# Optimization experiments

Hardware: AMD Instinct MI355X
Metric: run time of the kernel (lower is better)

The kernel has to match this reference:

```python
import jax, jax.numpy as jnp
import numpy as np

N = 50000      # nodes per type
E = 200000     # edges per relation
H, D = 4, 64   # heads, per-head dim
C = H * D      # hidden = hc_graph * heads = 256
L = 3          # num_hops (HGTConv layers)
HC_LIN, HC_TASK = 256, 128
OUT_DIMS = (3, 3, 3, 5, 1, 1, 8)  # ptr_l1/l2/l3, leaf_category, signed, floating, size


def setup_inputs() -> dict:
    key = jax.random.key(0)
    ks = jax.random.split(key, 24)
    f = lambda k, s: jax.random.normal(k, s, dtype=jnp.float32) * 0.05
    ri = lambda k: jax.random.randint(k, (E,), 0, N, dtype=jnp.int32)
    return {
        "xe": f(ks[0], (N, C)),
        "xs": f(ks[1], (N, C)),
        "ee_src": ri(ks[2]), "ee_dst": ri(ks[3]),
        "es_src": ri(ks[4]), "es_dst": ri(ks[5]),
        "se_src": ri(ks[6]), "se_dst": ri(ks[7]),
        # per-layer, per-node-type projections (2 node types)
        "Wk": f(ks[8], (L, 2, C, C)),
        "Wq": f(ks[9], (L, 2, C, C)),
        "Wv": f(ks[10], (L, 2, C, C)),
        "Wa": f(ks[11], (L, 2, C, C)),
        "skip": jnp.ones((L, 2), dtype=jnp.float32),
        # per-layer, per-relation attention/message transforms (3 relations)
        "Arel": f(ks[12], (L, 3, H, D, D)),
        "Mrel": f(ks[13], (L, 3, H, D, D)),
        "mu": jnp.ones((L, 3, H), dtype=jnp.float32),
        # shared linear stack + 7 task heads (final out padded to 8, sliced per head)
        "Wsh": f(ks[14], (2, HC_LIN, HC_LIN)),
        "bsh": jnp.zeros((2, HC_LIN), dtype=jnp.float32),
        "Wt1": f(ks[15], (7, HC_LIN, HC_TASK)),
        "bt1": jnp.zeros((7, HC_TASK), dtype=jnp.float32),
        "Wt2": f(ks[16], (7, HC_TASK, 8)),
        "bt2": jnp.zeros((7, 8), dtype=jnp.float32),
    }


def _seg_softmax(scores, seg, n):
    m = jax.ops.segment_max(scores, seg, num_segments=n)
    e = jnp.exp(scores - m[seg])
    s = jax.ops.segment_sum(e, seg, num_segments=n)
    return e / (s[seg] + 1e-16)


def _hgt_forward(xe, xs, ee_src, ee_dst, es_src, es_dst, se_src, se_dst,
                 Wk, Wq, Wv, Wa, skip, Arel, Mrel, mu, Wsh, bsh, Wt1, bt1, Wt2, bt2):
    inv_sqrt_d = 1.0 / jnp.sqrt(jnp.float32(D))

    def rel(k_src, v_src, q_dst, src, dst, A, M, m):
        kt = jnp.einsum('ehd,hdf->ehf', k_src[src], A)          # [E,H,D]
        score = (q_dst[dst] * kt).sum(-1) * (m * inv_sqrt_d)    # [E,H]
        msg = jnp.einsum('ehd,hdf->ehf', v_src[src], M)         # [E,H,D]
        return score, msg

    for l in range(L):
        ke = (xe @ Wk[l, 0]).reshape(N, H, D)
        qe = (xe @ Wq[l, 0]).reshape(N, H, D)
        ve = (xe @ Wv[l, 0]).reshape(N, H, D)
        ks_ = (xs @ Wk[l, 1]).reshape(N, H, D)
        qs = (xs @ Wq[l, 1]).reshape(N, H, D)
        vs = (xs @ Wv[l, 1]).reshape(N, H, D)

        s0, m0 = rel(ke, ve, qe, ee_src, ee_dst, Arel[l, 0], Mrel[l, 0], mu[l, 0])  # expr->expr
        s1, m1 = rel(ke, ve, qs, es_src, es_dst, Arel[l, 1], Mrel[l, 1], mu[l, 1])  # expr->stmt
        s2, m2 = rel(ks_, vs, qe, se_src, se_dst, Arel[l, 2], Mrel[l, 2], mu[l, 2])  # stmt->expr

        # destination 'expr': softmax over all incoming edges (rel0 + rel2)
        sc_e = jnp.concatenate([s0, s2], axis=0)
        ms_e = jnp.concatenate([m0, m2], axis=0)
        dst_e = jnp.concatenate([ee_dst, se_dst], axis=0)
        a_e = _seg_softmax(sc_e, dst_e, N)
        agg_e = jax.ops.segment_sum(a_e[..., None] * ms_e, dst_e, num_segments=N).reshape(N, C)

        # destination 'stmt': only rel1
        a_s = _seg_softmax(s1, es_dst, N)
        agg_s = jax.ops.segment_sum(a_s[..., None] * m1, es_dst, num_segments=N).reshape(N, C)

        be = jax.nn.sigmoid(skip[l, 0])
        bs = jax.nn.sigmoid(skip[l, 1])
        xe = be * (jax.nn.gelu(agg_e, approximate=False) @ Wa[l, 0]) + (1.0 - be) * xe
        xs = bs * (jax.nn.gelu(agg_s, approximate=False) @ Wa[l, 1]) + (1.0 - bs) * xs

    # shared linear stack on 'expr' nodes
    h = xe
    for i in range(Wsh.shape[0]):
        h = jax.nn.relu(h @ Wsh[i] + bsh[i])

    # 7 task heads: hidden layer + final (padded to 8 outputs, sliced per head)
    t = jax.nn.relu(jnp.einsum('nc,kct->knt', h, Wt1) + bt1[:, None, :])  # [7,N,HC_TASK]
    o = jnp.einsum('knt,kto->kno', t, Wt2) + bt2[:, None, :]              # [7,N,8]
    outs = [o[i, :, :d] for i, d in enumerate(OUT_DIMS)]
    return jnp.concatenate(outs, axis=-1)  # [N, 24]


def reference(xe, xs, ee_src, ee_dst, es_src, es_dst, se_src, se_dst,
              Wk, Wq, Wv, Wa, skip, Arel, Mrel, mu, Wsh, bsh, Wt1, bt1, Wt2, bt2):
    return _hgt_forward(xe, xs, ee_src, ee_dst, es_src, es_dst, se_src, se_dst,
                        Wk, Wq, Wv, Wa, skip, Arel, Mrel, mu, Wsh, bsh, Wt1, bt1, Wt2, bt2)
```

## Files before the change

### kernel.cpp

```cpp
#include <hip/hip_runtime.h>
#include <hip/hip_fp16.h>
#include <cmath>


#define CDIM 256
#define AR_R (256 * 256)

using f16x8 = __attribute__((ext_vector_type(8))) _Float16;
using f16x4 = __attribute__((ext_vector_type(4))) _Float16;
using f16x2 = __attribute__((ext_vector_type(2))) _Float16;
using f32x4 = __attribute__((ext_vector_type(4))) float;

__device__ __forceinline__ float gelu_f(float x) {
    return 0.5f * x * (1.0f + erff(x * 0.70710678118654752f));
}

__device__ __forceinline__ float dot4f(const f16x4 a, const f16x4 b) {
#if __has_builtin(__builtin_amdgcn_fdot2)
    f16x2 al = {a[0], a[1]}, ah = {a[2], a[3]};
    f16x2 bl = {b[0], b[1]}, bh = {b[2], b[3]};
    float r = __builtin_amdgcn_fdot2(al, bl, 0.0f, false);
    return __builtin_amdgcn_fdot2(ah, bh, r, false);
#else
    return (float)a[0] * (float)b[0] + (float)a[1] * (float)b[1] +
           (float)a[2] * (float)b[2] + (float)a[3] * (float)b[3];
#endif
}

__global__ __launch_bounds__(256) void zero_k(int* __restrict__ p, size_t n) {
    size_t i = (size_t)blockIdx.x * blockDim.x + threadIdx.x;
    const size_t stride = (size_t)gridDim.x * blockDim.x;
    for (; i < n; i += stride) p[i] = 0;
}

__global__ __launch_bounds__(256) void cvt_k(const float* __restrict__ in,
                                             _Float16* __restrict__ out,
                                             size_t n4) {
    size_t i = (size_t)blockIdx.x * blockDim.x + threadIdx.x;
    const size_t stride = (size_t)gridDim.x * blockDim.x;
    for (; i < n4; i += stride) {
        const float4 v = ((const float4*)in)[i];
        f16x4 o;
        o[0] = (_Float16)v.x; o[1] = (_Float16)v.y;
        o[2] = (_Float16)v.z; o[3] = (_Float16)v.w;
        ((f16x4*)out)[i] = o;
    }
}

__device__ __forceinline__ void cvtT_dev(const float* __restrict__ W,
                                         _Float16* __restrict__ dst) {
    const int o = blockIdx.x, c = threadIdx.x;
    dst[(size_t)o * 256 + c] = (_Float16)W[(size_t)c * 256 + o];
}

__device__ __forceinline__ void foldT_dev(const float* __restrict__ Wbase,
                                          const float* __restrict__ T,
                                          _Float16* __restrict__ dst) {
    __shared__ float row[256];
    const int c = blockIdx.x, t = threadIdx.x;
    row[t] = Wbase[(size_t)c * 256 + t];
    __syncthreads();
    const int h = t >> 6, f = t & 63;
    const float* Th = T + h * 4096;
    float acc = 0.f;
#pragma unroll 8
    for (int d = 0; d < 64; ++d) acc += row[h * 64 + d] * Th[d * 64 + f];
    dst[(size_t)t * 256 + c] = (_Float16)acc;
}

__global__ __launch_bounds__(256) void prep_layer_k(
    const float* __restrict__ Wk, const float* __restrict__ Wq,
    const float* __restrict__ Wv, const float* __restrict__ Wa,
    const float* __restrict__ Arel, const float* __restrict__ Mrel, int l,
    _Float16* __restrict__ arena) {
    const size_t CC = 65536, HDD = 16384;
    _Float16* L = arena + (size_t)l * 10 * AR_R;
    const float* Wk0 = Wk + (l * 2 + 0) * CC;
    const float* Wk1 = Wk + (l * 2 + 1) * CC;
    const float* Wv0 = Wv + (l * 2 + 0) * CC;
    const float* Wv1 = Wv + (l * 2 + 1) * CC;
    switch (blockIdx.y) {
        case 0: cvtT_dev(Wq + (l * 2 + 0) * CC, L); break;
        case 1: foldT_dev(Wk0, Arel + (l * 3 + 0) * HDD, L + 1 * AR_R); break;
        case 2: foldT_dev(Wk0, Arel + (l * 3 + 1) * HDD, L + 2 * AR_R); break;
        case 3: cvtT_dev(Wq + (l * 2 + 1) * CC, L + 3 * AR_R); break;
        case 4: foldT_dev(Wk1, Arel + (l * 3 + 2) * HDD, L + 4 * AR_R); break;
        case 5: foldT_dev(Wv0, Mrel + (l * 3 + 0) * HDD, L + 5 * AR_R); break;
        case 6: foldT_dev(Wv0, Mrel + (l * 3 + 1) * HDD, L + 6 * AR_R); break;
        case 7: foldT_dev(Wv1, Mrel + (l * 3 + 2) * HDD, L + 7 * AR_R); break;
        case 8: cvtT_dev(Wa + (l * 2 + 0) * CC, L + 8 * AR_R); break;
        case 9: cvtT_dev(Wa + (l * 2 + 1) * CC, L + 9 * AR_R); break;
    }
}

__global__ __launch_bounds__(256) void prep_stack_k(const float* __restrict__ Wsh,
                                                    _Float16* __restrict__ SA) {
    cvtT_dev(Wsh + (size_t)blockIdx.y * 65536, SA + (size_t)blockIdx.y * AR_R);
}

__global__ __launch_bounds__(256) void prep_heads_k(const float* __restrict__ Wt1,
                                                    _Float16* __restrict__ HA) {
    const int o = blockIdx.x, k = blockIdx.y, c = threadIdx.x;
    HA[(size_t)(k * 128 + o) * 256 + c] =
        (_Float16)Wt1[(size_t)k * 256 * 128 + (size_t)c * 128 + o];
}

template <int EPI, bool SPLIT>
__device__ __forceinline__ void gemm_body(
    const _Float16* __restrict__ A, const _Float16* __restrict__ Bt,
    _Float16* __restrict__ C, int M, int Nc, int bn, size_t bufStride,
    const float* __restrict__ bias, const float* __restrict__ skipv,
    _Float16* As, _Float16* Bs) {
    const int tid = threadIdx.x;
    const int bm = blockIdx.x * 128;
    const int wave = tid >> 6, lane = tid & 63;
    const int wm = (wave >> 1) * 64, wn = (wave & 1) * 64;
    const int l15 = lane & 15, g = lane >> 4;
    const int srow = tid >> 3;
    const int sbyte = (tid & 7) * 16;

    f32x4 acc[4][4] = {};

    for (int k0 = 0; k0 < 256; k0 += 64) {
        __syncthreads();
#pragma unroll
        for (int p = 0; p < 4; ++p) {
            const int r = p * 32 + srow;
            int gr = bm + r; if (gr >= M) gr = M - 1;
            const f16x8 av = *(const f16x8*)((const char*)A +
                                             ((size_t)gr * 256 + k0) * 2 + sbyte);
            const f16x8 bv = *(const f16x8*)((const char*)Bt +
                                             ((size_t)(bn + r) * 256 + k0) * 2 + sbyte);
            const int wb = sbyte ^ ((r & 7) << 4);
            *(f16x8*)((char*)As + r * 128 + wb) = av;
            *(f16x8*)((char*)Bs + r * 128 + wb) = bv;
        }
        __syncthreads();
#pragma unroll
        for (int sub = 0; sub < 2; ++sub) {
            f16x8 af[4], bf[4];
#pragma unroll
            for (int i = 0; i < 4; ++i) {
                const int ra = wm + i * 16 + l15;
                const int rb = wn + i * 16 + l15;
                const int ka = (sub * 64 + g * 16) ^ ((ra & 7) << 4);
                const int kb = (sub * 64 + g * 16) ^ ((rb & 7) << 4);
                af[i] = *(const f16x8*)((const char*)As + ra * 128 + ka);
                bf[i] = *(const f16x8*)((const char*)Bs + rb * 128 + kb);
            }
#pragma unroll
            for (int mi = 0; mi < 4; ++mi)
#pragma unroll
                for (int ni = 0; ni < 4; ++ni)
                    acc[mi][ni] = __builtin_amdgcn_mfma_f32_16x16x32_f16(
                        af[mi], bf[ni], acc[mi][ni], 0, 0, 0);
        }
    }

    float be = 0.f, ombe = 0.f;
    if (EPI == 1) {
        const float s = skipv[0];
        be = 1.0f / (1.0f + expf(-s));
        ombe = 1.0f - be;
    }
#pragma unroll
    for (int mi = 0; mi < 4; ++mi) {
#pragma unroll
        for (int r = 0; r < 4; ++r) {
            const int row = bm + wm + mi * 16 + g * 4 + r;
            if (row >= M) continue;
#pragma unroll
            for (int ni = 0; ni < 4; ++ni) {
                const int colg = bn + wn + ni * 16 + l15;
                float v = acc[mi][ni][r];
                size_t idx;
                if (SPLIT)
                    idx = (size_t)(colg >> 8) * bufStride + (size_t)row * 256 +
                          (colg & 255);
                else
                    idx = (size_t)row * Nc + colg;
                if (EPI == 1) v = be * v + ombe * (float)C[idx];
                if (EPI == 2) v = fmaxf(v + bias[colg], 0.f);
                C[idx] = (_Float16)v;
            }
        }
    }
}

template <int EPI, bool SPLIT>
__global__ __launch_bounds__(256) void gemm_h(
    const _Float16* __restrict__ A, const _Float16* __restrict__ Bt,
    _Float16* __restrict__ C, int M, int Nc, size_t bufStride,
    const float* __restrict__ bias, const float* __restrict__ skipv) {
    __shared__ _Float16 As[128 * 64];
    __shared__ _Float16 Bs[128 * 64];
    gemm_body<EPI, SPLIT>(A, Bt, C, M, Nc, blockIdx.y * 128, bufStride, bias,
                          skipv, As, Bs);
}

__global__ __launch_bounds__(256) void update2_k(
    const _Float16* __restrict__ aggE, const _Float16* __restrict__ aggS,
    const _Float16* __restrict__ WaT0, const _Float16* __restrict__ WaT1,
    _Float16* __restrict__ xeH, _Float16* __restrict__ xsH,
    const float* __restrict__ skipb, int M) {
    __shared__ _Float16 As[128 * 64];
    __shared__ _Float16 Bs[128 * 64];
    const int sel = blockIdx.y >> 1;
    const int bn = (blockIdx.y & 1) * 128;
    if (sel == 0)
        gemm_body<1, false>(aggE, WaT0, xeH, M, 256, bn, 0, nullptr, skipb, As, Bs);
    else
        gemm_body<1, false>(aggS, WaT1, xsH, M, 256, bn, 0, nullptr, skipb + 1, As, Bs);
}

__global__ __launch_bounds__(256) void hist3_k(const int* __restrict__ d0,
                                               const int* __restrict__ d1,
                                               const int* __restrict__ d2,
                                               int* __restrict__ cnt, int N,
                                               int E) {
    const int i = blockIdx.x * 256 + threadIdx.x;
    if (i >= E) return;
    const int r = blockIdx.y;
    const int* d = r == 0 ? d0 : r == 1 ? d1 : d2;
    atomicAdd(&cnt[(size_t)r * N + d[i]], 1);
}

__global__ __launch_bounds__(1024) void scan3_k(const int* __restrict__ cnt,
                                                int* __restrict__ rp, int N) {
    __shared__ int sums[1024];
    const int r = blockIdx.y;
    const int* c = cnt + (size_t)r * N;
    int* o = rp + (size_t)r * (N + 1);
    const int tid = threadIdx.x;
    const int chunk = (N + 1023) / 1024;
    const int lo = min(tid * chunk, N), hi = min(lo + chunk, N);
    int s = 0;
    for (int i = lo; i < hi; ++i) s += c[i];
    sums[tid] = s;
    __syncthreads();
    for (int off = 1; off < 1024; off <<= 1) {
        const int v = (tid >= off) ? sums[tid - off] : 0;
        __syncthreads();
        sums[tid] += v;
        __syncthreads();
    }
    int run = (tid == 0) ? 0 : sums[tid - 1];
    for (int i = lo; i < hi; ++i) { o[i] = run; run += c[i]; }
    if (tid == 1023) o[N] = run;
}

__global__ __launch_bounds__(256) void scatter3_k(
    const int* __restrict__ d0, const int* __restrict__ d1,
    const int* __restrict__ d2, const int* __restrict__ s0_,
    const int* __restrict__ s1_, const int* __restrict__ s2_,
    const int* __restrict__ rp, int* __restrict__ fill,
    int* __restrict__ colsrc, int N, int E) {
    const int i = blockIdx.x * 256 + threadIdx.x;
    if (i >= E) return;
    const int r = blockIdx.y;
    const int* d = r == 0 ? d0 : r == 1 ? d1 : d2;
    const int* s = r == 0 ? s0_ : r == 1 ? s1_ : s2_;
    const int dd = d[i];
    const int p = rp[(size_t)r * (N + 1) + dd] + atomicAdd(&fill[(size_t)r * N + dd], 1);
    colsrc[(size_t)r * E + p] = s[i];
}

__device__ __forceinline__ void score_rel(
    const f16x4 qv, const _Float16* __restrict__ kA,
    const int* __restrict__ cs, int beg, int end, float scale,
    float* __restrict__ sc, int lane, int h, float& m) {
    int i = beg;
    for (; i + 1 < end; i += 2) {
        const int sA = cs[i], sB = cs[i + 1];
        const f16x4 k0 = *(const f16x4*)&kA[(size_t)sA * 256 + lane * 4];
        const f16x4 k1 = *(const f16x4*)&kA[(size_t)sB * 256 + lane * 4];
        float p0 = dot4f(qv, k0), p1 = dot4f(qv, k1);
        p0 += __shfl_xor(p0, 1); p1 += __shfl_xor(p1, 1);
        p0 += __shfl_xor(p0, 2); p1 += __shfl_xor(p1, 2);
        p0 += __shfl_xor(p0, 4); p1 += __shfl_xor(p1, 4);
        p0 += __shfl_xor(p0, 8); p1 += __shfl_xor(p1, 8);
        const float v0 = p0 * scale, v1 = p1 * scale;
        if ((lane & 15) == 0) {
            sc[(size_t)i * 4 + h] = v0;
            sc[(size_t)(i + 1) * 4 + h] = v1;
        }
        m = fmaxf(m, fmaxf(v0, v1));
    }
    if (i < end) {
        const int sA = cs[i];
        const f16x4 k0 = *(const f16x4*)&kA[(size_t)sA * 256 + lane * 4];
        float p0 = dot4f(qv, k0);
        p0 += __shfl_xor(p0, 1); p0 += __shfl_xor(p0, 2);
        p0 += __shfl_xor(p0, 4); p0 += __shfl_xor(p0, 8);
        const float v0 = p0 * scale;
        if ((lane & 15) == 0) sc[(size_t)i * 4 + h] = v0;
        m = fmaxf(m, v0);
    }
}

__global__ __launch_bounds__(256) void score3_k(
    const _Float16* __restrict__ qe, const _Float16* __restrict__ kA0,
    const _Float16* __restrict__ kA1, const _Float16* __restrict__ qs,
    const _Float16* __restrict__ kA2, const int* __restrict__ rp,
    const int* __restrict__ colsrc, const float* __restrict__ muL,
    float* __restrict__ sc, float* __restrict__ mx_e,
    float* __restrict__ mx_s, int N, int E) {
    const int wid = (blockIdx.x * blockDim.x + threadIdx.x) >> 6;
    if (wid >= N) return;
    const int lane = threadIdx.x & 63;
    const int h = lane >> 4;
    const size_t E4 = (size_t)E * 4;
    float m = -1e30f;
    if (blockIdx.y == 0) {
        const f16x4 qv = *(const f16x4*)&qe[(size_t)wid * 256 + lane * 4];
        score_rel(qv, kA0, colsrc, rp[wid], rp[wid + 1],
                  muL[0 * 4 + h] * 0.125f, sc, lane, h, m);
        const int* rp2 = rp + 2 * (N + 1);
        score_rel(qv, kA2, colsrc + 2 * (size_t)E, rp2[wid], rp2[wid + 1],
                  muL[2 * 4 + h] * 0.125f, sc + 2 * E4, lane, h, m);
        if ((lane & 15) == 0) mx_e[(size_t)wid * 4 + h] = m;
    } else {
        const f16x4 qv = *(const f16x4*)&qs[(size_t)wid * 256 + lane * 4];
        const int* rp1 = rp + (N + 1);
        score_rel(qv, kA1, colsrc + (size_t)E, rp1[wid], rp1[wid + 1],
                  muL[1 * 4 + h] * 0.125f, sc + E4, lane, h, m);
        if ((lane & 15) == 0) mx_s[(size_t)wid * 4 + h] = m;
    }
}

__device__ __forceinline__ void agg_rel(const float* __restrict__ sc,
                                        const _Float16* __restrict__ vM,
                                        const int* __restrict__ cs, int beg,
                                        int end, float m, float dinv, int lane,
                                        int h, float4& acc) {
    int i = beg;
    for (; i + 1 < end; i += 2) {
        const int sA = cs[i], sB = cs[i + 1];
        const float w0 = expf(sc[(size_t)i * 4 + h] - m) * dinv;
        const float w1 = expf(sc[(size_t)(i + 1) * 4 + h] - m) * dinv;
        const f16x4 v0 = *(const f16x4*)&vM[(size_t)sA * 256 + lane * 4];
        const f16x4 v1 = *(const f16x4*)&vM[(size_t)sB * 256 + lane * 4];
        acc.x += w0 * (float)v0[0] + w1 * (float)v1[0];
        acc.y += w0 * (float)v0[1] + w1 * (float)v1[1];
        acc.z += w0 * (float)v0[2] + w1 * (float)v1[2];
        acc.w += w0 * (float)v0[3] + w1 * (float)v1[3];
    }
    if (i < end) {
        const int sA = cs[i];
        const float w0 = expf(sc[(size_t)i * 4 + h] - m) * dinv;
        const f16x4 v0 = *(const f16x4*)&vM[(size_t)sA * 256 + lane * 4];
        acc.x += w0 * (float)v0[0]; acc.y += w0 * (float)v0[1];
        acc.z += w0 * (float)v0[2]; acc.w += w0 * (float)v0[3];
    }
}

__global__ __launch_bounds__(256) void agg3_k(
    const float* __restrict__ sc, const _Float16* __restrict__ vM0,
    const _Float16* __restrict__ vM1, const _Float16* __restrict__ vM2,
    const int* __restrict__ rp, const int* __restrict__ colsrc,
    const float* __restrict__ mx_e, const float* __restrict__ mx_s,
    _Float16* __restrict__ outE, _Float16* __restrict__ outS, int N, int E) {
    const int wid = (blockIdx.x * blockDim.x + threadIdx.x) >> 6;
    if (wid >= N) return;
    const int lane = threadIdx.x & 63;
    const int hHi = lane >> 4, hLo = lane & 3, sl = lane >> 2;
    const size_t E4 = (size_t)E * 4;
    float4 acc = make_float4(0.f, 0.f, 0.f, 0.f);
    if (blockIdx.y == 0) {
        const float mLo = mx_e[(size_t)wid * 4 + hLo];
        const float mHi = mx_e[(size_t)wid * 4 + hHi];
        const int b0 = rp[wid], e0 = rp[wid + 1];
        const int* rp2 = rp + 2 * (N + 1);
        const int b2 = rp2[wid], e2 = rp2[wid + 1];
        const float* sc2 = sc + 2 * E4;
        float dl = 0.f;
        for (int i = b0 + sl; i < e0; i += 16)
            dl += expf(sc[(size_t)i * 4 + hLo] - mLo);
        for (int i = b2 + sl; i < e2; i += 16)
            dl += expf(sc2[(size_t)i * 4 + hLo] - mLo);
        dl += __shfl_xor(dl, 4); dl += __shfl_xor(dl, 8);
        dl += __shfl_xor(dl, 16); dl += __shfl_xor(dl, 32);
        const float dinv = 1.0f / (__shfl(dl, hHi) + 1e-16f);
        agg_rel(sc, vM0, colsrc, b0, e0, mHi, dinv, lane, hHi, acc);
        agg_rel(sc2, vM2, colsrc + 2 * (size_t)E, b2, e2, mHi, dinv, lane, hHi,
                acc);
        f16x4 o;
        o[0] = (_Float16)gelu_f(acc.x); o[1] = (_Float16)gelu_f(acc.y);
        o[2] = (_Float16)gelu_f(acc.z); o[3] = (_Float16)gelu_f(acc.w);
        *(f16x4*)&outE[(size_t)wid * 256 + lane * 4] = o;
    } else {
        const float mLo = mx_s[(size_t)wid * 4 + hLo];
        const float mHi = mx_s[(size_t)wid * 4 + hHi];
        const int* rp1 = rp + (N + 1);
        const int b1 = rp1[wid], e1 = rp1[wid + 1];
        const float* sc1 = sc + E4;
        float dl = 0.f;
        for (int i = b1 + sl; i < e1; i += 16)
            dl += expf(sc1[(size_t)i * 4 + hLo] - mLo);
        dl += __shfl_xor(dl, 4); dl += __shfl_xor(dl, 8);
        dl += __shfl_xor(dl, 16); dl += __shfl_xor(dl, 32);
        const float dinv = 1.0f / (__shfl(dl, hHi) + 1e-16f);
        agg_rel(sc1, vM1, colsrc + (size_t)E, b1, e1, mHi, dinv, lane, hHi,
                acc);
        f16x4 o;
        o[0] = (_Float16)gelu_f(acc.x); o[1] = (_Float16)gelu_f(acc.y);
        o[2] = (_Float16)gelu_f(acc.z); o[3] = (_Float16)gelu_f(acc.w);
        *(f16x4*)&outS[(size_t)wid * 256 + lane * 4] = o;
    }
}

__global__ __launch_bounds__(256) void head2_k(const _Float16* __restrict__ t,
                                               const float* __restrict__ Wt2,
                                               const float* __restrict__ bt2,
                                               float* __restrict__ out, int M) {
    const int k = blockIdx.y;
    __shared__ float Ws[128 * 8];
    __shared__ float bs[8];
    const int tid = threadIdx.x;
    const float* W2 = Wt2 + (size_t)k * 1024;
    for (int i = tid; i < 1024; i += 256) Ws[i] = W2[i];
    if (tid < 8) bs[tid] = bt2[k * 8 + tid];
    __syncthreads();
    const int OFFA[7] = {0, 3, 6, 9, 14, 15, 16};
    const int DIMSA[7] = {3, 3, 3, 5, 1, 1, 8};
    const int nl = tid >> 3, o = tid & 7;
    const int n = blockIdx.x * 32 + nl;
    if (n >= M) return;
    const _Float16* tr = &t[(size_t)n * 896 + k * 128];
    float acc = bs[o];
#pragma unroll 8
    for (int d = 0; d < 128; ++d) acc += (float)tr[d] * Ws[d * 8 + o];
    if (o < DIMSA[k]) out[(size_t)n * 24 + OFFA[k] + o] = acc;
}


extern "C" void kernel_launch(void* const* d_in, const int* in_sizes, int n_in,
                              void* d_out, int out_size, void* d_ws,
                              size_t ws_size, hipStream_t stream) {
    const float* xe_in = (const float*)d_in[0];
    const float* xs_in = (const float*)d_in[1];
    const int* ee_src = (const int*)d_in[2];
    const int* ee_dst = (const int*)d_in[3];
    const int* es_src = (const int*)d_in[4];
    const int* es_dst = (const int*)d_in[5];
    const int* se_src = (const int*)d_in[6];
    const int* se_dst = (const int*)d_in[7];
    const float* Wk = (const float*)d_in[8];
    const float* Wq = (const float*)d_in[9];
    const float* Wv = (const float*)d_in[10];
    const float* Wa = (const float*)d_in[11];
    const float* skip = (const float*)d_in[12];
    const float* Arel = (const float*)d_in[13];
    const float* Mrel = (const float*)d_in[14];
    const float* mu = (const float*)d_in[15];
    const float* Wsh = (const float*)d_in[16];
    const float* bsh = (const float*)d_in[17];
    const float* Wt1 = (const float*)d_in[18];
    const float* bt1 = (const float*)d_in[19];
    const float* Wt2 = (const float*)d_in[20];
    const float* bt2 = (const float*)d_in[21];
    float* out = (float*)d_out;

    const int N = in_sizes[0] / CDIM;
    const int E = in_sizes[2];
    const size_t NC = (size_t)N * CDIM;
    const size_t E4 = (size_t)E * 4;
    const size_t N4 = (size_t)N * 4;

    const size_t halfs = 7 * NC + 32 * (size_t)AR_R + 7 * 32768;
    const size_t floats = 3 * E4 + 2 * N4;
    const size_t ints = 3 * (size_t)(N + 1) + 3 * (size_t)E + 3 * (size_t)N;
    const size_t need = halfs * 2 + floats * 4 + ints * 4;
    if (ws_size < need) return;

    _Float16* xeH = (_Float16*)d_ws;
    _Float16* xsH = xeH + NC;
    _Float16* Hb = xsH + NC;
    _Float16* H1 = Hb;
    _Float16* H2 = Hb + NC;
    _Float16* H3 = Hb + 2 * NC;
    _Float16* H4 = Hb + 3 * NC;
    _Float16* H5 = Hb + 4 * NC;
    _Float16* arena = Hb + 5 * NC;
    _Float16* SA = arena + (size_t)30 * AR_R;
    _Float16* HA = SA + (size_t)2 * AR_R;
    float* sc = (float*)(HA + (size_t)7 * 32768);
    float* mx_e = sc + 3 * E4;
    float* mx_s = mx_e + N4;
    int* rp = (int*)(mx_s + N4);
    int* colsrc = rp + 3 * (size_t)(N + 1);
    int* cnt = colsrc + 3 * (size_t)E;

    const int gx = (N + 127) / 128;
    const dim3 e3((E + 255) / 256, 3);
    const int wave_blocks = (N + 3) / 4;
    const int zc_blocks = (3 * N + 255) / 256;

    zero_k<<<zc_blocks, 256, 0, stream>>>(cnt, 3 * (size_t)N);
    hist3_k<<<e3, 256, 0, stream>>>(ee_dst, es_dst, se_dst, cnt, N, E);
    scan3_k<<<dim3(1, 3), 1024, 0, stream>>>(cnt, rp, N);
    zero_k<<<zc_blocks, 256, 0, stream>>>(cnt, 3 * (size_t)N);
    scatter3_k<<<e3, 256, 0, stream>>>(ee_dst, es_dst, se_dst, ee_src, es_src,
                                       se_src, rp, cnt, colsrc, N, E);

    for (int l = 0; l < 3; ++l)
        prep_layer_k<<<dim3(256, 10), 256, 0, stream>>>(Wk, Wq, Wv, Wa, Arel,
                                                        Mrel, l, arena);
    prep_stack_k<<<dim3(256, 2), 256, 0, stream>>>(Wsh, SA);
    prep_heads_k<<<dim3(128, 7), 256, 0, stream>>>(Wt1, HA);

    cvt_k<<<1024, 256, 0, stream>>>(xe_in, xeH, NC / 4);
    cvt_k<<<1024, 256, 0, stream>>>(xs_in, xsH, NC / 4);

    for (int l = 0; l < 3; ++l) {
        _Float16* L = arena + (size_t)l * 10 * AR_R;
        gemm_h<0, true><<<dim3(gx, 6), 256, 0, stream>>>(
            xeH, L, H1, N, 768, NC, nullptr, nullptr);
        gemm_h<0, true><<<dim3(gx, 4), 256, 0, stream>>>(
            xsH, L + 3 * AR_R, H4, N, 512, NC, nullptr, nullptr);
        score3_k<<<dim3(wave_blocks, 2), 256, 0, stream>>>(
            H1, H2, H3, H4, H5, rp, colsrc, mu + l * 12, sc, mx_e, mx_s, N, E);
        gemm_h<0, true><<<dim3(gx, 4), 256, 0, stream>>>(
            xeH, L + 5 * AR_R, H2, N, 512, NC, nullptr, nullptr);
        gemm_h<0, false><<<dim3(gx, 2), 256, 0, stream>>>(
            xsH, L + 7 * AR_R, H5, N, 256, 0, nullptr, nullptr);
        agg3_k<<<dim3(wave_blocks, 2), 256, 0, stream>>>(
            sc, H2, H3, H5, rp, colsrc, mx_e, mx_s, H1, H4, N, E);
        update2_k<<<dim3(gx, 4), 256, 0, stream>>>(
            H1, H4, L + 8 * AR_R, L + 9 * AR_R, xeH, xsH, skip + l * 2, N);
    }

    gemm_h<2, false><<<dim3(gx, 2), 256, 0, stream>>>(xeH, SA, H5, N, 256, 0,
                                                      bsh, nullptr);
    gemm_h<2, false><<<dim3(gx, 2), 256, 0, stream>>>(H5, SA + AR_R, xsH, N,
                                                      256, 0, bsh + 256, nullptr);
    gemm_h<2, false><<<dim3(gx, 7), 256, 0, stream>>>(xsH, HA, Hb, N, 896, 0,
                                                      bt1, nullptr);
    head2_k<<<dim3((N + 31) / 32, 7), 256, 0, stream>>>(Hb, Wt2, bt2, out, N);
}
```

Before: 1.251 ms.

## Process four edges per wave with 16-byte row loads in score/agg kernels

Score and aggregation kernels now split each wave into four 16-lane groups. Each group handles a different incoming edge and each lane loads 16 halves via two 16-byte vector loads, instead of the whole wave walking edges serially with 8-byte loads. Partial dot products are reduced within 4 lanes, and the max and accumulators are combined across groups with shuffles before writing. This raises memory-level parallelism for the gather but adds cross-group reductions and more accumulator registers.

```diff
diff --git a/kernel.cpp b/kernel.cpp
--- a/kernel.cpp
+++ b/kernel.cpp
@@ -15,16 +15,19 @@
     return 0.5f * x * (1.0f + erff(x * 0.70710678118654752f));
 }
 
-__device__ __forceinline__ float dot4f(const f16x4 a, const f16x4 b) {
+__device__ __forceinline__ float dot8f(const f16x8 a, const f16x8 b, float r) {
 #if __has_builtin(__builtin_amdgcn_fdot2)
-    f16x2 al = {a[0], a[1]}, ah = {a[2], a[3]};
-    f16x2 bl = {b[0], b[1]}, bh = {b[2], b[3]};
-    float r = __builtin_amdgcn_fdot2(al, bl, 0.0f, false);
-    return __builtin_amdgcn_fdot2(ah, bh, r, false);
+#pragma unroll
+    for (int t = 0; t < 4; ++t) {
+        f16x2 av = {a[2 * t], a[2 * t + 1]};
+        f16x2 bv = {b[2 * t], b[2 * t + 1]};
+        r = __builtin_amdgcn_fdot2(av, bv, r, false);
+    }
 #else
-    return (float)a[0] * (float)b[0] + (float)a[1] * (float)b[1] +
-           (float)a[2] * (float)b[2] + (float)a[3] * (float)b[3];
+#pragma unroll
+    for (int t = 0; t < 8; ++t) r += (float)a[t] * (float)b[t];
 #endif
+    return r;
 }
 
 __global__ __launch_bounds__(256) void zero_k(int* __restrict__ p, size_t n) {
@@ -265,36 +268,23 @@
     colsrc[(size_t)r * E + p] = s[i];
 }
 
-__device__ __forceinline__ void score_rel(
-    const f16x4 qv, const _Float16* __restrict__ kA,
-    const int* __restrict__ cs, int beg, int end, float scale,
-    float* __restrict__ sc, int lane, int h, float& m) {
-    int i = beg;
-    for (; i + 1 < end; i += 2) {
-        const int sA = cs[i], sB = cs[i + 1];
-        const f16x4 k0 = *(const f16x4*)&kA[(size_t)sA * 256 + lane * 4];
-        const f16x4 k1 = *(const f16x4*)&kA[(size_t)sB * 256 + lane * 4];
-        float p0 = dot4f(qv, k0), p1 = dot4f(qv, k1);
-        p0 += __shfl_xor(p0, 1); p1 += __shfl_xor(p1, 1);
-        p0 += __shfl_xor(p0, 2); p1 += __shfl_xor(p1, 2);
-        p0 += __shfl_xor(p0, 4); p1 += __shfl_xor(p1, 4);
-        p0 += __shfl_xor(p0, 8); p1 += __shfl_xor(p1, 8);
-        const float v0 = p0 * scale, v1 = p1 * scale;
-        if ((lane & 15) == 0) {
-            sc[(size_t)i * 4 + h] = v0;
-            sc[(size_t)(i + 1) * 4 + h] = v1;
-        }
-        m = fmaxf(m, fmaxf(v0, v1));
-    }
-    if (i < end) {
-        const int sA = cs[i];
-        const f16x4 k0 = *(const f16x4*)&kA[(size_t)sA * 256 + lane * 4];
-        float p0 = dot4f(qv, k0);
-        p0 += __shfl_xor(p0, 1); p0 += __shfl_xor(p0, 2);
-        p0 += __shfl_xor(p0, 4); p0 += __shfl_xor(p0, 8);
-        const float v0 = p0 * scale;
-        if ((lane & 15) == 0) sc[(size_t)i * 4 + h] = v0;
-        m = fmaxf(m, v0);
+__device__ __forceinline__ void score_rel_g(
+    const f16x8 q0, const f16x8 q1, const _Float16* __restrict__ kA,
+    const int* __restrict__ cs, int beg, int end, float scl,
+    float* __restrict__ sc, int grp, int j, float& m) {
+    for (int i = beg + grp; i < end; i += 4) {
+        const int s = cs[i];
+        const _Float16* row = &kA[(size_t)s * 256 + j * 16];
+        const f16x8 k0 = *(const f16x8*)row;
+        const f16x8 k1 = *(const f16x8*)(row + 8);
+        float p = dot8f(q1, k1, dot8f(q0, k0, 0.f));
+        p += __shfl_xor(p, 1);
+        p += __shfl_xor(p, 2);
+        const float v = p * scl;
+        if ((j & 3) == 0) {
+            sc[(size_t)i * 4 + (j >> 2)] = v;
+            m = fmaxf(m, v);
+        }
     }
 }
 
@@ -308,49 +298,48 @@
     const int wid = (blockIdx.x * blockDim.x + threadIdx.x) >> 6;
     if (wid >= N) return;
     const int lane = threadIdx.x & 63;
-    const int h = lane >> 4;
+    const int grp = lane >> 4, j = lane & 15, h = j >> 2;
     const size_t E4 = (size_t)E * 4;
     float m = -1e30f;
     if (blockIdx.y == 0) {
-        const f16x4 qv = *(const f16x4*)&qe[(size_t)wid * 256 + lane * 4];
-        score_rel(qv, kA0, colsrc, rp[wid], rp[wid + 1],
-                  muL[0 * 4 + h] * 0.125f, sc, lane, h, m);
+        const _Float16* qrow = &qe[(size_t)wid * 256 + j * 16];
+        const f16x8 q0 = *(const f16x8*)qrow;
+        const f16x8 q1 = *(const f16x8*)(qrow + 8);
+        score_rel_g(q0, q1, kA0, colsrc, rp[wid], rp[wid + 1],
+                    muL[0 * 4 + h] * 0.125f, sc, grp, j, m);
         const int* rp2 = rp + 2 * (N + 1);
-        score_rel(qv, kA2, colsrc + 2 * (size_t)E, rp2[wid], rp2[wid + 1],
-                  muL[2 * 4 + h] * 0.125f, sc + 2 * E4, lane, h, m);
-        if ((lane & 15) == 0) mx_e[(size_t)wid * 4 + h] = m;
+        score_rel_g(q0, q1, kA2, colsrc + 2 * (size_t)E, rp2[wid], rp2[wid + 1],
+                    muL[2 * 4 + h] * 0.125f, sc + 2 * E4, grp, j, m);
+        m = fmaxf(m, __shfl_xor(m, 16));
+        m = fmaxf(m, __shfl_xor(m, 32));
+        if (grp == 0 && (j & 3) == 0) mx_e[(size_t)wid * 4 + h] = m;
     } else {
-        const f16x4 qv = *(const f16x4*)&qs[(size_t)wid * 256 + lane * 4];
+        const _Float16* qrow = &qs[(size_t)wid * 256 + j * 16];
+        const f16x8 q0 = *(const f16x8*)qrow;
+        const f16x8 q1 = *(const f16x8*)(qrow + 8);
         const int* rp1 = rp + (N + 1);
-        score_rel(qv, kA1, colsrc + (size_t)E, rp1[wid], rp1[wid + 1],
-                  muL[1 * 4 + h] * 0.125f, sc + E4, lane, h, m);
-        if ((lane & 15) == 0) mx_s[(size_t)wid * 4 + h] = m;
-    }
-}
-
-__device__ __forceinline__ void agg_rel(const float* __restrict__ sc,
-                                        const _Float16* __restrict__ vM,
-                                        const int* __restrict__ cs, int beg,
-                                        int end, float m, float dinv, int lane,
-                                        int h, float4& acc) {
-    int i = beg;
-    for (; i + 1 < end; i += 2) {
-        const int sA = cs[i], sB = cs[i + 1];
-        const float w0 = expf(sc[(size_t)i * 4 + h] - m) * dinv;
-        const float w1 = expf(sc[(size_t)(i + 1) * 4 + h] - m) * dinv;
-        const f16x4 v0 = *(const f16x4*)&vM[(size_t)sA * 256 + lane * 4];
-        const f16x4 v1 = *(const f16x4*)&vM[(size_t)sB * 256 + lane * 4];
-        acc.x += w0 * (float)v0[0] + w1 * (float)v1[0];
-        acc.y += w0 * (float)v0[1] + w1 * (float)v1[1];
-        acc.z += w0 * (float)v0[2] + w1 * (float)v1[2];
-        acc.w += w0 * (float)v0[3] + w1 * (float)v1[3];
-    }
-    if (i < end) {
-        const int sA = cs[i];
-        const float w0 = expf(sc[(size_t)i * 4 + h] - m) * dinv;
-        const f16x4 v0 = *(const f16x4*)&vM[(size_t)sA * 256 + lane * 4];
-        acc.x += w0 * (float)v0[0]; acc.y += w0 * (float)v0[1];
-        acc.z += w0 * (float)v0[2]; acc.w += w0 * (float)v0[3];
+        score_rel_g(q0, q1, kA1, colsrc + (size_t)E, rp1[wid], rp1[wid + 1],
+                    muL[1 * 4 + h] * 0.125f, sc + E4, grp, j, m);
+        m = fmaxf(m, __shfl_xor(m, 16));
+        m = fmaxf(m, __shfl_xor(m, 32));
+        if (grp == 0 && (j & 3) == 0) mx_s[(size_t)wid * 4 + h] = m;
+    }
+}
+
+__device__ __forceinline__ void agg_rel_g(
+    const float* __restrict__ sc, const _Float16* __restrict__ vM,
+    const int* __restrict__ cs, int beg, int end, float mh, float dinv,
+    int grp, int j, int h, float* accf) {
+    for (int i = beg + grp; i < end; i += 4) {
+        const int s = cs[i];
+        const float w = expf(sc[(size_t)i * 4 + h] - mh) * dinv;
+        const _Float16* row = &vM[(size_t)s * 256 + j * 16];
+        const f16x8 v0 = *(const f16x8*)row;
+        const f16x8 v1 = *(const f16x8*)(row + 8);
+#pragma unroll
+        for (int t = 0; t < 8; ++t) accf[t] += w * (float)v0[t];
+#pragma unroll
+        for (int t = 0; t < 8; ++t) accf[8 + t] += w * (float)v1[t];
     }
 }
 
@@ -363,12 +352,13 @@
     const int wid = (blockIdx.x * blockDim.x + threadIdx.x) >> 6;
     if (wid >= N) return;
     const int lane = threadIdx.x & 63;
-    const int hHi = lane >> 4, hLo = lane & 3, sl = lane >> 2;
+    const int grp = lane >> 4, j = lane & 15, h = j >> 2;
+    const int hLo = lane & 3, sl = lane >> 2;
     const size_t E4 = (size_t)E * 4;
-    float4 acc = make_float4(0.f, 0.f, 0.f, 0.f);
+    float accf[16] = {};
     if (blockIdx.y == 0) {
         const float mLo = mx_e[(size_t)wid * 4 + hLo];
-        const float mHi = mx_e[(size_t)wid * 4 + hHi];
+        const float mh = mx_e[(size_t)wid * 4 + h];
         const int b0 = rp[wid], e0 = rp[wid + 1];
         const int* rp2 = rp + 2 * (N + 1);
         const int b2 = rp2[wid], e2 = rp2[wid + 1];
@@ -380,17 +370,28 @@
             dl += expf(sc2[(size_t)i * 4 + hLo] - mLo);
         dl += __shfl_xor(dl, 4); dl += __shfl_xor(dl, 8);
         dl += __shfl_xor(dl, 16); dl += __shfl_xor(dl, 32);
-        const float dinv = 1.0f / (__shfl(dl, hHi) + 1e-16f);
-        agg_rel(sc, vM0, colsrc, b0, e0, mHi, dinv, lane, hHi, acc);
-        agg_rel(sc2, vM2, colsrc + 2 * (size_t)E, b2, e2, mHi, dinv, lane, hHi,
-                acc);
-        f16x4 o;
-        o[0] = (_Float16)gelu_f(acc.x); o[1] = (_Float16)gelu_f(acc.y);
-        o[2] = (_Float16)gelu_f(acc.z); o[3] = (_Float16)gelu_f(acc.w);
-        *(f16x4*)&outE[(size_t)wid * 256 + lane * 4] = o;
+        const float dinv = 1.0f / (__shfl(dl, h) + 1e-16f);
+        agg_rel_g(sc, vM0, colsrc, b0, e0, mh, dinv, grp, j, h, accf);
+        agg_rel_g(sc2, vM2, colsrc + 2 * (size_t)E, b2, e2, mh, dinv, grp, j,
+                  h, accf);
+#pragma unroll
+        for (int t = 0; t < 16; ++t) {
+            accf[t] += __shfl_xor(accf[t], 16);
+            accf[t] += __shfl_xor(accf[t], 32);
+        }
+        if (grp == 0) {
+            f16x8 o0, o1;
+#pragma unroll
+            for (int t = 0; t < 8; ++t) o0[t] = (_Float16)gelu_f(accf[t]);
+#pragma unroll
+            for (int t = 0; t < 8; ++t) o1[t] = (_Float16)gelu_f(accf[8 + t]);
+            _Float16* dst = &outE[(size_t)wid * 256 + j * 16];
+            *(f16x8*)dst = o0;
+            *(f16x8*)(dst + 8) = o1;
+        }
     } else {
         const float mLo = mx_s[(size_t)wid * 4 + hLo];
-        const float mHi = mx_s[(size_t)wid * 4 + hHi];
+        const float mh = mx_s[(size_t)wid * 4 + h];
         const int* rp1 = rp + (N + 1);
         const int b1 = rp1[wid], e1 = rp1[wid + 1];
         const float* sc1 = sc + E4;
@@ -399,13 +400,24 @@
             dl += expf(sc1[(size_t)i * 4 + hLo] - mLo);
         dl += __shfl_xor(dl, 4); dl += __shfl_xor(dl, 8);
         dl += __shfl_xor(dl, 16); dl += __shfl_xor(dl, 32);
-        const float dinv = 1.0f / (__shfl(dl, hHi) + 1e-16f);
-        agg_rel(sc1, vM1, colsrc + (size_t)E, b1, e1, mHi, dinv, lane, hHi,
-                acc);
-        f16x4 o;
-        o[0] = (_Float16)gelu_f(acc.x); o[1] = (_Float16)gelu_f(acc.y);
-        o[2] = (_Float16)gelu_f(acc.z); o[3] = (_Float16)gelu_f(acc.w);
-        *(f16x4*)&outS[(size_t)wid * 256 + lane * 4] = o;
+        const float dinv = 1.0f / (__shfl(dl, h) + 1e-16f);
+        agg_rel_g(sc1, vM1, colsrc + (size_t)E, b1, e1, mh, dinv, grp, j, h,
+                  accf);
+#pragma unroll
+        for (int t = 0; t < 16; ++t) {
+            accf[t] += __shfl_xor(accf[t], 16);
+            accf[t] += __shfl_xor(accf[t], 32);
+        }
+        if (grp == 0) {
+            f16x8 o0, o1;
+#pragma unroll
+            for (int t = 0; t < 8; ++t) o0[t] = (_Float16)gelu_f(accf[t]);
+#pragma unroll
+            for (int t = 0; t < 8; ++t) o1[t] = (_Float16)gelu_f(accf[8 + t]);
+            _Float16* dst = &outS[(size_t)wid * 256 + j * 16];
+            *(f16x8*)dst = o0;
+            *(f16x8*)(dst + 8) = o1;
+        }
     }
 }
 
```

Result: faster. 1.202 ms (-3.9%).
